# Performance work log

Measured on AMD Instinct MI355X. Metric: run time of the kernel, lower is better.

Reference implementation:

```python
import jax, jax.numpy as jnp
import numpy as np

B, N, C = 8, 3136, 128
NUM_HEADS = 2
HEAD_DIM = C // NUM_HEADS  # 64
SCALE = HEAD_DIM ** -0.5


def setup_inputs() -> dict:
    key = jax.random.key(0)
    ks = jax.random.split(key, 10)
    s = 0.02
    return {
        "x": jax.random.normal(ks[0], (B, N, C), jnp.float32),
        "H": 56,
        "W": 56,
        "relative_pos": jax.random.normal(ks[1], (NUM_HEADS, N, N), jnp.float32),
        "Wq": jax.random.normal(ks[2], (C, C), jnp.float32) * s,
        "bq": jnp.zeros((C,), jnp.float32),
        "Wk": jax.random.normal(ks[3], (C, C), jnp.float32) * s,
        "bk": jnp.zeros((C,), jnp.float32),
        "Wv": jax.random.normal(ks[4], (C, C), jnp.float32) * s,
        "bv": jnp.zeros((C,), jnp.float32),
        "Wp": jax.random.normal(ks[5], (C, C), jnp.float32) * s,
        "bp": jnp.zeros((C,), jnp.float32),
    }


def reference(x, H, W, relative_pos, Wq, bq, Wk, bk, Wv, bv, Wp, bp):
    # x: [B, N, C]; sr_ratio == 1 path of Attention.forward
    b, n, c = x.shape
    h, dh = NUM_HEADS, HEAD_DIM
    # q/k/v projections -> [B, h, N, dh] (torch Linear: x @ W.T + b)
    q = (x @ Wq.T + bq).reshape(b, n, h, dh).transpose(0, 2, 1, 3)
    k = (x @ Wk.T + bk).reshape(b, n, h, dh).transpose(0, 2, 1, 3)
    v = (x @ Wv.T + bv).reshape(b, n, h, dh).transpose(0, 2, 1, 3)
    # scores with additive relative-position bias: [B, h, N, N]
    attn = jnp.einsum("bhnd,bhmd->bhnm", q, k) * SCALE + relative_pos[None]
    attn = jax.nn.softmax(attn, axis=-1)
    # AV -> [B, N, C]
    out = jnp.einsum("bhnm,bhmd->bhnd", attn, v).transpose(0, 2, 1, 3).reshape(b, n, c)
    return out @ Wp.T + bp
```

## Files before the change

kernel.cpp:

```cpp
#include <hip/hip_runtime.h>
#include <hip/hip_fp16.h>

#define N_TOK 3136
#define DH 64
#define NHEAD 2
#define CDIM 128
#define BATCH 8
#define NT 49
#define QK_SCALE 0.18033688011112f
#define LOG2E 1.4426950408889634f

typedef __attribute__((ext_vector_type(8))) short bf16x8;
typedef __attribute__((ext_vector_type(8))) _Float16 f16x8;
typedef __attribute__((ext_vector_type(2))) _Float16 f16x2;
typedef __attribute__((ext_vector_type(2))) __fp16 fp16x2;
typedef __attribute__((ext_vector_type(4))) float f32x4;
typedef __attribute__((ext_vector_type(16))) float f32x16;
typedef __attribute__((ext_vector_type(4))) unsigned short u16x4;
typedef __attribute__((ext_vector_type(4))) unsigned int u32x4;

__device__ __forceinline__ unsigned short f2bf(float f) {
  unsigned int u = __float_as_uint(f);
  u += 0x7fffu + ((u >> 16) & 1u);
  return (unsigned short)(u >> 16);
}

#define MFMA16(a, b, c)    __builtin_amdgcn_mfma_f32_16x16x32_bf16(a, b, c, 0, 0, 0)
#define MFMA32_BF(a, b, c) __builtin_amdgcn_mfma_f32_32x32x16_bf16(a, b, c, 0, 0, 0)
#define MFMA32_F16(a, b, c) __builtin_amdgcn_mfma_f32_32x32x16_f16(a, b, c, 0, 0, 0)

__device__ __forceinline__ void plswap(unsigned& a, unsigned& b) {
  asm volatile("v_permlane32_swap_b32 %0, %1" : "+v"(a), "+v"(b));
}

__device__ __forceinline__ f16x2 pkrtz(float a, float b) {
  union { fp16x2 p; f16x2 h; } cv;
  cv.p = __builtin_amdgcn_cvt_pkrtz(a, b);
  return cv.h;
}

__device__ __forceinline__ float dot2acc(f16x2 pr, float acc) {
#if __has_builtin(__builtin_amdgcn_fdot2)
  union { f16x2 h; fp16x2 p; } c; c.h = pr;
  fp16x2 ones = {(__fp16)1.0f, (__fp16)1.0f};
  return __builtin_amdgcn_fdot2(c.p, ones, acc, false);
#else
  return acc + (float)pr[0] + (float)pr[1];
#endif
}

__device__ __forceinline__ void stage_w(const float* __restrict__ W,
                                        unsigned short (*wsh)[136], int tid) {
  const float4* Wv4 = (const float4*)W;
#pragma unroll
  for (int i = 0; i < 16; ++i) {
    int f = tid + i * 256;
    float4 v = Wv4[f];
    int row = f >> 5, col = (f & 31) << 2;
    u16x4 pk = { f2bf(v.x), f2bf(v.y), f2bf(v.z), f2bf(v.w) };
    *(u16x4*)&wsh[row][col] = pk;
  }
}

__device__ __forceinline__ void mfma_block(const unsigned short (*xs)[136],
                                           const unsigned short (*wsh)[136],
                                           int w, int lk, int lg, f32x4* acc) {
#pragma unroll
  for (int nf = 0; nf < 8; ++nf) acc[nf] = (f32x4){0.f, 0.f, 0.f, 0.f};
#pragma unroll
  for (int kk = 0; kk < 4; ++kk) {
    bf16x8 a = *(const bf16x8*)&xs[w * 16 + lk][kk * 32 + 8 * lg];
#pragma unroll
    for (int nf = 0; nf < 8; ++nf) {
      bf16x8 b = *(const bf16x8*)&wsh[nf * 16 + lk][kk * 32 + 8 * lg];
      acc[nf] = MFMA16(a, b, acc[nf]);
    }
  }
}

__global__ __launch_bounds__(256)
void proj_qkv(const float* __restrict__ x,
              const float* __restrict__ Wq, const float* __restrict__ bq,
              const float* __restrict__ Wk, const float* __restrict__ bk,
              const float* __restrict__ Wv, const float* __restrict__ bv,
              unsigned short* __restrict__ qo, unsigned short* __restrict__ ko,
              unsigned short* __restrict__ vo)
{
  __shared__ __align__(16) unsigned short xs[64][136];
  __shared__ __align__(16) unsigned short wsh[128][136];
  const int tid = threadIdx.x;
  const int m0 = blockIdx.x * 64;
  const int w = tid >> 6, l = tid & 63;
  const int lk = l & 15, lg = l >> 4;

  {
    const float4* Xv = (const float4*)(x + (size_t)m0 * CDIM);
#pragma unroll
    for (int i = 0; i < 8; ++i) {
      int f = tid + i * 256;
      float4 v = Xv[f];
      int row = f >> 5, col = (f & 31) << 2;
      u16x4 pk = { f2bf(v.x), f2bf(v.y), f2bf(v.z), f2bf(v.w) };
      *(u16x4*)&xs[row][col] = pk;
    }
  }
  stage_w(Wq, wsh, tid);
  __syncthreads();

  f32x4 acc[8];

  mfma_block(xs, wsh, w, lk, lg, acc);
#pragma unroll
  for (int reg = 0; reg < 4; ++reg) {
    int row = m0 + w * 16 + 4 * lg + reg;
    int bb = row / N_TOK, tok = row - bb * N_TOK;
#pragma unroll
    for (int nf = 0; nf < 8; ++nf) {
      int col = nf * 16 + lk;
      float val = (acc[nf][reg] + bq[col]) * QK_SCALE;
      qo[((size_t)(bb * NHEAD + (nf >> 2)) * N_TOK + tok) * DH + (col & 63)] = f2bf(val);
    }
  }
  __syncthreads();

  stage_w(Wk, wsh, tid);
  __syncthreads();
  mfma_block(xs, wsh, w, lk, lg, acc);
#pragma unroll
  for (int reg = 0; reg < 4; ++reg) {
    int row = m0 + w * 16 + 4 * lg + reg;
    int bb = row / N_TOK, tok = row - bb * N_TOK;
#pragma unroll
    for (int nf = 0; nf < 8; ++nf) {
      int col = nf * 16 + lk;
      float val = acc[nf][reg] + bk[col];
      ko[((size_t)(bb * NHEAD + (nf >> 2)) * N_TOK + tok) * DH + (col & 63)] = f2bf(val);
    }
  }
  __syncthreads();

  stage_w(Wv, wsh, tid);
  __syncthreads();
  mfma_block(xs, wsh, w, lk, lg, acc);
#pragma unroll
  for (int reg = 0; reg < 4; ++reg) {
    int row = m0 + w * 16 + 4 * lg + reg;
    int bb = row / N_TOK, tok = row - bb * N_TOK;
#pragma unroll
    for (int nf = 0; nf < 8; ++nf) {
      int col = nf * 16 + lk;
      float val = acc[nf][reg] + bv[col];
      size_t idx = ((size_t)(bb * NHEAD + (nf >> 2)) * DH + (col & 63)) * N_TOK + tok;
      vo[idx] = __half_as_ushort(__float2half(val));
    }
  }
}

__global__ __launch_bounds__(256)
void exp_rp(const float* __restrict__ rp, __half* __restrict__ E)
{
  const int hkt = blockIdx.x;
  const int h = hkt / NT, kt = hkt % NT;
  const int q0 = blockIdx.y * 64;
  const int t = threadIdx.x;
  const int kp = t & 63;
  const int qi = t >> 6;

  const int ct = kp >> 5;
  const int kpp = kp & 31;
  const int hi = (kpp >> 2) & 1;
  const int r = (kpp & 3) + ((kpp >> 3) << 2);
  const int didx = hi * 32 + ct * 16 + r;

  const float* src = rp + ((size_t)h * N_TOK + q0) * N_TOK + kt * 64 + kp;
  __half* dst = E + (((size_t)h * NT + kt) * N_TOK + q0) * 64 + didx;

#pragma unroll
  for (int i = 0; i < 16; ++i) {
    int q = qi * 16 + i;
    float v = __expf(src[(size_t)q * N_TOK]);
    dst[(size_t)q * 64] = __float2half(v);
  }
}

__global__ __launch_bounds__(256)
void attn32(const unsigned short* __restrict__ q_ws,
            const unsigned short* __restrict__ k_ws,
            const unsigned short* __restrict__ v_ws,
            const __half* __restrict__ E,
            unsigned short* __restrict__ attn_out)
{
  __shared__ __align__(16) unsigned short LDSU[2][9216];

  const int b = blockIdx.x, qt = blockIdx.y, head = blockIdx.z;
  const int tid = threadIdx.x;
  const int w = tid >> 6, l = tid & 63;
  const int lq = l & 31, hi = l >> 5;

  const size_t bh = ((size_t)b * NHEAD + head) * N_TOK;
  const unsigned short* Kp = k_ws + bh * DH;
  const _Float16* Vt = (const _Float16*)v_ws + bh * DH;

  int qg = qt * 128 + w * 32 + lq;
  if (qg > N_TOK - 1) qg = N_TOK - 1;

  bf16x8 qf[4];
  {
    const unsigned short* qrow = q_ws + (bh + (size_t)qg) * DH + 8 * hi;
#pragma unroll
    for (int ks = 0; ks < 4; ++ks) qf[ks] = *(const bf16x8*)(qrow + 16 * ks);
  }

  const int kr0 = tid >> 3, ku = tid & 7;
  const int kofs = kr0 * 72 + ku * 8;
  const int gk0 = kr0 * DH + ku * 8, gk1 = gk0 + 32 * DH;
  const int gvt0 = kr0 * N_TOK + ku * 8, gvt1 = gvt0 + 32 * N_TOK;

  const __half* Eb = E + (((size_t)head * NT) * N_TOK + (size_t)qg) * DH + hi * 32;

  float lsum = 0.f;
  f32x16 o0, o1;
#pragma unroll
  for (int i = 0; i < 16; ++i) { o0[i] = 0.f; o1[i] = 0.f; }

  bf16x8 kpreA = *(const bf16x8*)(Kp + gk0);
  bf16x8 kpreB = *(const bf16x8*)(Kp + gk1);
  f16x8 vpreA = *(const f16x8*)(Vt + gvt0);
  f16x8 vpreB = *(const f16x8*)(Vt + gvt1);

  u32x4 EwA[4], EwB[4];
  {
    const u32x4* ep = (const u32x4*)Eb;
#pragma unroll
    for (int f = 0; f < 4; ++f) EwA[f] = ep[f];
  }

  *(bf16x8*)&LDSU[0][kofs] = kpreA;
  *(bf16x8*)&LDSU[0][kofs + 32 * 72] = kpreB;
  *(f16x8*)&LDSU[0][4608 + kofs] = vpreA;
  *(f16x8*)&LDSU[0][4608 + kofs + 32 * 72] = vpreB;
  {
    const unsigned short* kn = Kp + (size_t)64 * DH;
    const _Float16* vn = Vt + 64;
    kpreA = *(const bf16x8*)(kn + gk0);
    kpreB = *(const bf16x8*)(kn + gk1);
    vpreA = *(const f16x8*)(vn + gvt0);
    vpreB = *(const f16x8*)(vn + gvt1);
  }
  asm volatile("s_waitcnt lgkmcnt(0)" ::: "memory");
  __builtin_amdgcn_s_barrier();
  asm volatile("" ::: "memory");

#define ATTN_BODY(PH, KT, EW_CUR, EW_NXT, LAST)                               \
  {                                                                           \
    const unsigned short* Kb = &LDSU[PH][0];                                  \
    const unsigned short* Vb = &LDSU[PH][4608];                               \
    unsigned short* Kn = &LDSU[PH ^ 1][0];                                    \
    unsigned short* Vn = &LDSU[PH ^ 1][4608];                                 \
    if (!(LAST)) {                                         \
      const u32x4* ep = (const u32x4*)(Eb + (size_t)((KT) + 1) * (N_TOK * DH)); \
      _Pragma("unroll") for (int f = 0; f < 4; ++f) EW_NXT[f] = ep[f];        \
    }                                                                         \
                                                           \
    f32x16 s0, s1;                                                            \
    _Pragma("unroll") for (int i = 0; i < 16; ++i) { s0[i] = 0.f; s1[i] = 0.f; } \
    __builtin_amdgcn_s_setprio(1);                                            \
    _Pragma("unroll") for (int ks = 0; ks < 4; ++ks) {                        \
      bf16x8 kf0 = *(const bf16x8*)&Kb[lq * 72 + 16 * ks + 8 * hi];           \
      s0 = MFMA32_BF(kf0, qf[ks], s0);                                        \
      bf16x8 kf1 = *(const bf16x8*)&Kb[(32 + lq) * 72 + 16 * ks + 8 * hi];    \
      s1 = MFMA32_BF(kf1, qf[ks], s1);                                        \
    }                                                                         \
    __builtin_amdgcn_s_setprio(0);                                            \
    if (!(LAST)) {            \
      *(bf16x8*)&Kn[kofs] = kpreA;                                            \
      *(bf16x8*)&Kn[kofs + 32 * 72] = kpreB;                                  \
      *(f16x8*)&Vn[kofs] = vpreA;                                             \
      *(f16x8*)&Vn[kofs + 32 * 72] = vpreB;                                   \
      if ((KT) + 2 < NT) {                                                    \
        const unsigned short* kn2 = Kp + (size_t)((KT) + 2) * 64 * DH;        \
        const _Float16* vn2 = Vt + (size_t)((KT) + 2) * 64;                   \
        kpreA = *(const bf16x8*)(kn2 + gk0);                                  \
        kpreB = *(const bf16x8*)(kn2 + gk1);                                  \
        vpreA = *(const f16x8*)(vn2 + gvt0);                                  \
        vpreB = *(const f16x8*)(vn2 + gvt1);                                  \
      }                                                                       \
    }                                                                         \
                                \
    unsigned pw[16];                                                          \
    _Pragma("unroll") for (int f = 0; f < 4; ++f) {                           \
      int rb = (f & 1) * 8;                                                   \
      _Pragma("unroll") for (int i = 0; i < 4; ++i) {                         \
        float a = (f >> 1) ? s1[rb + 2 * i] : s0[rb + 2 * i];                 \
        float c = (f >> 1) ? s1[rb + 2 * i + 1] : s0[rb + 2 * i + 1];         \
        f16x2 pp = pkrtz(__builtin_amdgcn_exp2f(a), __builtin_amdgcn_exp2f(c)); \
        union { unsigned u; f16x2 h; } ec; ec.u = EW_CUR[f][i];               \
        f16x2 pr = pp * ec.h;                                                 \
        lsum = dot2acc(pr, lsum);                                             \
        union { f16x2 h; unsigned u; } pu; pu.h = pr;                         \
        pw[4 * f + i] = pu.u;                                                 \
      }                                                                       \
      plswap(pw[4 * f + 0], pw[4 * f + 2]);                                   \
      plswap(pw[4 * f + 1], pw[4 * f + 3]);                                   \
    }                                                                         \
                                                        \
    __builtin_amdgcn_s_setprio(1);                                            \
    _Pragma("unroll") for (int ks = 0; ks < 4; ++ks) {                        \
      union { unsigned u[4]; f16x8 v; } pf;                                   \
      _Pragma("unroll") for (int i = 0; i < 4; ++i) pf.u[i] = pw[4 * ks + i]; \
      f16x8 vf0 = *(const f16x8*)&Vb[lq * 72 + 16 * ks + 8 * hi];             \
      o0 = MFMA32_F16(vf0, pf.v, o0);                                         \
      f16x8 vf1 = *(const f16x8*)&Vb[(32 + lq) * 72 + 16 * ks + 8 * hi];      \
      o1 = MFMA32_F16(vf1, pf.v, o1);                                         \
    }                                                                         \
    __builtin_amdgcn_s_setprio(0);                                            \
    if (!(LAST)) {                                                            \
      asm volatile("s_waitcnt lgkmcnt(0)" ::: "memory");                      \
      __builtin_amdgcn_s_barrier();                                           \
      asm volatile("" ::: "memory");                                          \
    }                                                                         \
  }

  for (int kt2 = 0; kt2 < (NT - 1) / 2; ++kt2) {
    int kt = 2 * kt2;
    ATTN_BODY(0, kt, EwA, EwB, false);
    ATTN_BODY(1, kt + 1, EwB, EwA, false);
  }
  ATTN_BODY(0, NT - 1, EwA, EwB, true);
#undef ATTN_BODY

  lsum += __shfl_xor(lsum, 32, 64);
  float inv = 1.f / lsum;

  __syncthreads();
  unsigned short* Ot = &LDSU[0][0];
  const int orow = (w * 32 + lq) * 72;
#pragma unroll
  for (int dt = 0; dt < 2; ++dt) {
#pragma unroll
    for (int j = 0; j < 8; ++j) {
      float v0 = (dt ? o1[2 * j] : o0[2 * j]) * inv;
      float v1 = (dt ? o1[2 * j + 1] : o0[2 * j + 1]) * inv;
      unsigned pk;
      asm("v_cvt_pk_bf16_f32 %0, %1, %2" : "=v"(pk) : "v"(v0), "v"(v1));
      int d = ((2 * j) & 3) + 8 * ((2 * j) >> 2) + 4 * hi + 32 * dt;
      *(unsigned*)&Ot[orow + d] = pk;
    }
  }
  __syncthreads();
#pragma unroll
  for (int i = 0; i < 4; ++i) {
    int c = tid + 256 * i;
    int ql = c >> 3, du = c & 7;
    int tok = qt * 128 + ql;
    if (tok < N_TOK) {
      u32x4 val = *(const u32x4*)&Ot[ql * 72 + du * 8];
      *(u32x4*)&attn_out[((size_t)b * N_TOK + tok) * CDIM + head * DH + du * 8] = val;
    }
  }
}

template<bool IN_F32, int OMODE>
__global__ __launch_bounds__(256)
void proj_gemm(const void* __restrict__ Ain, const float* __restrict__ W,
               const float* __restrict__ bias, void* __restrict__ Out,
               float out_scale)
{
  __shared__ __align__(16) unsigned short xs[64][136];
  __shared__ __align__(16) unsigned short wsh[128][136];
  const int tid = threadIdx.x;
  const int m0 = blockIdx.x * 64;
  const int w = tid >> 6, l = tid & 63;
  const int lk = l & 15, lg = l >> 4;

  stage_w(W, wsh, tid);
  if (IN_F32) {
    const float4* Xv = (const float4*)((const float*)Ain + (size_t)m0 * CDIM);
#pragma unroll
    for (int i = 0; i < 8; ++i) {
      int f = tid + i * 256;
      float4 v = Xv[f];
      int row = f >> 5, col = (f & 31) << 2;
      u16x4 pk = { f2bf(v.x), f2bf(v.y), f2bf(v.z), f2bf(v.w) };
      *(u16x4*)&xs[row][col] = pk;
    }
  } else {
    const bf16x8* Xv = (const bf16x8*)((const unsigned short*)Ain + (size_t)m0 * CDIM);
#pragma unroll
    for (int i = 0; i < 4; ++i) {
      int c = tid + i * 256;
      bf16x8 v = Xv[c];
      int row = c >> 4, col = (c & 15) << 3;
      *(bf16x8*)&xs[row][col] = v;
    }
  }
  __syncthreads();

  f32x4 acc[8];
  mfma_block(xs, wsh, w, lk, lg, acc);

#pragma unroll
  for (int reg = 0; reg < 4; ++reg) {
    int row = m0 + w * 16 + 4 * lg + reg;
    int bb = row / N_TOK;
    int tok = row - bb * N_TOK;
#pragma unroll
    for (int nf = 0; nf < 8; ++nf) {
      int col = nf * 16 + lk;
      float val = (acc[nf][reg] + bias[col]) * out_scale;
      if (OMODE == 0) {
        ((float*)Out)[(size_t)row * CDIM + col] = val;
      } else {
        int head = nf >> 2;
        int d = col & 63;
        size_t idx = ((size_t)(bb * NHEAD + head) * N_TOK + tok) * DH + d;
        ((unsigned short*)Out)[idx] = f2bf(val);
      }
    }
  }
}

__global__ __launch_bounds__(256)
void attn_fallback(const unsigned short* __restrict__ q_ws,
                   const unsigned short* __restrict__ k_ws,
                   const unsigned short* __restrict__ v_ws,
                   const float* __restrict__ relpos,
                   unsigned short* __restrict__ attn_out)
{
  __shared__ __align__(16) unsigned short Ks[64][72];
  __shared__ __align__(16) unsigned short Vts[64][72];
  __shared__ __align__(16) unsigned short Ps[4][16][72];

  const int b = blockIdx.x, qt = blockIdx.y, head = blockIdx.z;
  const int tid = threadIdx.x;
  const int w = tid >> 6, l = tid & 63;
  const int lk = l & 15, lg = l >> 4;

  const size_t bh = ((size_t)b * NHEAD + head) * N_TOK;
  const unsigned short* Qp = q_ws + (bh + (size_t)qt * 64) * DH;
  const unsigned short* Kp = k_ws + bh * DH;
  const unsigned short* Vg = v_ws + bh * DH;

  bf16x8 qf0, qf1;
  {
    const unsigned short* qrow = Qp + (size_t)(w * 16 + lk) * DH + 8 * lg;
    qf0 = *(const bf16x8*)qrow;
    qf1 = *(const bf16x8*)(qrow + 32);
  }

  const int kr0 = tid >> 3;
  const int ku = (tid & 7) << 3;
  const int gk0 = kr0 * DH + ku;
  const int gk1 = gk0 + 32 * DH;
  const int vkey = tid & 63;
  const int vd0 = (tid >> 6) << 3;
  const int gv0 = vkey * DH + vd0;
  const int gv1 = gv0 + 32;

  const int qrow0 = qt * 64 + w * 16;
  const float* rpb = relpos + (size_t)head * N_TOK * N_TOK +
                     (size_t)(qrow0 + 4 * lg) * N_TOK + lk;

  float l_run[4] = {0.f, 0.f, 0.f, 0.f};
  f32x4 acc[4];
#pragma unroll
  for (int nf = 0; nf < 4; ++nf) acc[nf] = (f32x4){0.f, 0.f, 0.f, 0.f};

  bf16x8 kpreA = *(const bf16x8*)(Kp + gk0);
  bf16x8 kpreB = *(const bf16x8*)(Kp + gk1);
  bf16x8 vpreA = *(const bf16x8*)(Vg + gv0);
  bf16x8 vpreB = *(const bf16x8*)(Vg + gv1);

  for (int kt = 0; kt < NT; ++kt) {
    float rp[4][4];
#pragma unroll
    for (int r = 0; r < 4; ++r)
#pragma unroll
      for (int ct = 0; ct < 4; ++ct)
        rp[ct][r] = rpb[(size_t)r * N_TOK + kt * 64 + ct * 16];

    asm volatile("s_waitcnt lgkmcnt(0)" ::: "memory");
    __builtin_amdgcn_s_barrier();
    asm volatile("" ::: "memory");

    *(bf16x8*)&Ks[kr0][ku] = kpreA;
    *(bf16x8*)&Ks[kr0 + 32][ku] = kpreB;
#pragma unroll
    for (int j = 0; j < 8; ++j) Vts[vd0 + j][vkey] = ((const unsigned short*)&vpreA)[j];
#pragma unroll
    for (int j = 0; j < 8; ++j) Vts[vd0 + 32 + j][vkey] = ((const unsigned short*)&vpreB)[j];

    if (kt + 1 < NT) {
      const unsigned short* kn = Kp + (size_t)(kt + 1) * 64 * DH;
      const unsigned short* vn = Vg + (size_t)(kt + 1) * 64 * DH;
      kpreA = *(const bf16x8*)(kn + gk0);
      kpreB = *(const bf16x8*)(kn + gk1);
      vpreA = *(const bf16x8*)(vn + gv0);
      vpreB = *(const bf16x8*)(vn + gv1);
    }

    asm volatile("s_waitcnt lgkmcnt(0)" ::: "memory");
    __builtin_amdgcn_s_barrier();
    asm volatile("" ::: "memory");

    f32x4 s[4];
#pragma unroll
    for (int ct = 0; ct < 4; ++ct) s[ct] = (f32x4){0.f, 0.f, 0.f, 0.f};
#pragma unroll
    for (int ct = 0; ct < 4; ++ct) {
      bf16x8 kb0 = *(const bf16x8*)&Ks[ct * 16 + lk][8 * lg];
      s[ct] = MFMA16(qf0, kb0, s[ct]);
      bf16x8 kb1 = *(const bf16x8*)&Ks[ct * 16 + lk][32 + 8 * lg];
      s[ct] = MFMA16(qf1, kb1, s[ct]);
    }

#pragma unroll
    for (int ct = 0; ct < 4; ++ct) {
      float p0 = __builtin_amdgcn_exp2f(fmaf(rp[ct][0], LOG2E, s[ct][0]));
      float p1 = __builtin_amdgcn_exp2f(fmaf(rp[ct][1], LOG2E, s[ct][1]));
      float p2 = __builtin_amdgcn_exp2f(fmaf(rp[ct][2], LOG2E, s[ct][2]));
      float p3 = __builtin_amdgcn_exp2f(fmaf(rp[ct][3], LOG2E, s[ct][3]));
      l_run[0] += p0; l_run[1] += p1; l_run[2] += p2; l_run[3] += p3;
      Ps[w][4 * lg + 0][ct * 16 + lk] = f2bf(p0);
      Ps[w][4 * lg + 1][ct * 16 + lk] = f2bf(p1);
      Ps[w][4 * lg + 2][ct * 16 + lk] = f2bf(p2);
      Ps[w][4 * lg + 3][ct * 16 + lk] = f2bf(p3);
    }

    bf16x8 pa0 = *(const bf16x8*)&Ps[w][lk][8 * lg];
    bf16x8 pa1 = *(const bf16x8*)&Ps[w][lk][32 + 8 * lg];
#pragma unroll
    for (int nf = 0; nf < 4; ++nf) {
      bf16x8 vb0 = *(const bf16x8*)&Vts[nf * 16 + lk][8 * lg];
      acc[nf] = MFMA16(pa0, vb0, acc[nf]);
      bf16x8 vb1 = *(const bf16x8*)&Vts[nf * 16 + lk][32 + 8 * lg];
      acc[nf] = MFMA16(pa1, vb1, acc[nf]);
    }
  }

#pragma unroll
  for (int m = 1; m <= 8; m <<= 1)
#pragma unroll
    for (int r = 0; r < 4; ++r)
      l_run[r] += __shfl_xor(l_run[r], m, 64);

#pragma unroll
  for (int r = 0; r < 4; ++r) {
    int tok = qrow0 + 4 * lg + r;
    float inv = 1.f / l_run[r];
#pragma unroll
    for (int nf = 0; nf < 4; ++nf) {
      attn_out[((size_t)b * N_TOK + tok) * CDIM + head * DH + nf * 16 + lk] =
          f2bf(acc[nf][r] * inv);
    }
  }
}

extern "C" void kernel_launch(void* const* d_in, const int* in_sizes, int n_in,
                              void* d_out, int out_size, void* d_ws, size_t ws_size,
                              hipStream_t stream) {
  (void)in_sizes; (void)n_in; (void)out_size;
  const float* x      = (const float*)d_in[0];
  const float* relpos = (const float*)d_in[3];
  const float* Wq = (const float*)d_in[4];  const float* bq = (const float*)d_in[5];
  const float* Wk = (const float*)d_in[6];  const float* bk = (const float*)d_in[7];
  const float* Wv = (const float*)d_in[8];  const float* bv = (const float*)d_in[9];
  const float* Wp = (const float*)d_in[10]; const float* bp = (const float*)d_in[11];

  const size_t QKV_ELEMS = (size_t)BATCH * NHEAD * N_TOK * DH;
  const size_t E_ELEMS   = (size_t)NHEAD * NT * N_TOK * DH;
  unsigned short* q_ws  = (unsigned short*)d_ws;
  unsigned short* k_ws  = q_ws + QKV_ELEMS;
  unsigned short* v_ws  = k_ws + QKV_ELEMS;
  unsigned short* ao_ws = v_ws + QKV_ELEMS;
  __half* E_ws = (__half*)(ao_ws + QKV_ELEMS);

  const bool big = ws_size >= (4 * QKV_ELEMS + E_ELEMS) * sizeof(unsigned short);

  dim3 blk(256);
  const int MTILES = (BATCH * N_TOK) / 64;

  if (big) {
    proj_qkv<<<MTILES, blk, 0, stream>>>(x, Wq, bq, Wk, bk, Wv, bv, q_ws, k_ws, v_ws);
    exp_rp<<<dim3(NHEAD * NT, N_TOK / 64), blk, 0, stream>>>(relpos, E_ws);
    attn32<<<dim3(BATCH, (N_TOK + 127) / 128, NHEAD), blk, 0, stream>>>(
        q_ws, k_ws, v_ws, E_ws, ao_ws);
  } else {
    proj_gemm<true, 1><<<MTILES, blk, 0, stream>>>((const void*)x, Wq, bq, (void*)q_ws, QK_SCALE);
    proj_gemm<true, 1><<<MTILES, blk, 0, stream>>>((const void*)x, Wk, bk, (void*)k_ws, 1.f);
    proj_gemm<true, 1><<<MTILES, blk, 0, stream>>>((const void*)x, Wv, bv, (void*)v_ws, 1.f);
    attn_fallback<<<dim3(BATCH, N_TOK / 64, NHEAD), blk, 0, stream>>>(
        q_ws, k_ws, v_ws, relpos, ao_ws);
  }

  proj_gemm<false, 0><<<MTILES, blk, 0, stream>>>((const void*)ao_ws, Wp, bp, d_out, 1.f);
}
```

Before: 120.9 us.

## Merge QKV projection with exp(relpos) kernel and halve attention query tile

Folds the exp(relative_pos) precompute into the QKV projection kernel as extra blocks, removing one launch and letting both independent jobs run concurrently. The attention kernel drops from 256 threads and 128 queries per block to 128 threads and 64 queries, raising the grid from 25 to 49 query tiles per batch-head. This removes the padded last tile and improves load balance across CUs. In exchange, each block stages the same K/V tiles for half as many queries, doubling K/V LDS traffic per query, and each thread now issues four loads per tile instead of two.

```diff
diff --git a/kernel.cpp b/kernel.cpp
--- a/kernel.cpp
+++ b/kernel.cpp
@@ -7,6 +7,9 @@
 #define CDIM 128
 #define BATCH 8
 #define NT 49
+#define QT1 49
+#define MTILES ((BATCH * N_TOK) / 64)
+#define EXPBLKS (NHEAD * NT * (N_TOK / 64))
 #define QK_SCALE 0.18033688011112f
 #define LOG2E 1.4426950408889634f
 
@@ -79,16 +82,43 @@
 }
 
 __global__ __launch_bounds__(256)
-void proj_qkv(const float* __restrict__ x,
-              const float* __restrict__ Wq, const float* __restrict__ bq,
-              const float* __restrict__ Wk, const float* __restrict__ bk,
-              const float* __restrict__ Wv, const float* __restrict__ bv,
-              unsigned short* __restrict__ qo, unsigned short* __restrict__ ko,
-              unsigned short* __restrict__ vo)
+void pre_kernel(const float* __restrict__ x,
+                const float* __restrict__ Wq, const float* __restrict__ bq,
+                const float* __restrict__ Wk, const float* __restrict__ bk,
+                const float* __restrict__ Wv, const float* __restrict__ bv,
+                unsigned short* __restrict__ qo, unsigned short* __restrict__ ko,
+                unsigned short* __restrict__ vo,
+                const float* __restrict__ rp, __half* __restrict__ E)
 {
   __shared__ __align__(16) unsigned short xs[64][136];
   __shared__ __align__(16) unsigned short wsh[128][136];
   const int tid = threadIdx.x;
+
+  if (blockIdx.x >= MTILES) {
+    const int eb = blockIdx.x - MTILES;
+    const int hkt = eb % (NHEAD * NT);
+    const int q0 = (eb / (NHEAD * NT)) * 64;
+    const int h = hkt / NT, kt = hkt % NT;
+    const int kp = tid & 63;
+    const int qi = tid >> 6;
+
+    const int ct = kp >> 5;
+    const int kpp = kp & 31;
+    const int hi = (kpp >> 2) & 1;
+    const int r = (kpp & 3) + ((kpp >> 3) << 2);
+    const int didx = hi * 32 + ct * 16 + r;
+
+    const float* src = rp + ((size_t)h * N_TOK + q0) * N_TOK + kt * 64 + kp;
+    __half* dst = E + (((size_t)h * NT + kt) * N_TOK + q0) * 64 + didx;
+#pragma unroll
+    for (int i = 0; i < 16; ++i) {
+      int q = qi * 16 + i;
+      float v = __expf(src[(size_t)q * N_TOK]);
+      dst[(size_t)q * 64] = __float2half(v);
+    }
+    return;
+  }
+
   const int m0 = blockIdx.x * 64;
   const int w = tid >> 6, l = tid & 63;
   const int lk = l & 15, lg = l >> 4;
@@ -156,34 +186,7 @@
   }
 }
 
-__global__ __launch_bounds__(256)
-void exp_rp(const float* __restrict__ rp, __half* __restrict__ E)
-{
-  const int hkt = blockIdx.x;
-  const int h = hkt / NT, kt = hkt % NT;
-  const int q0 = blockIdx.y * 64;
-  const int t = threadIdx.x;
-  const int kp = t & 63;
-  const int qi = t >> 6;
-
-  const int ct = kp >> 5;
-  const int kpp = kp & 31;
-  const int hi = (kpp >> 2) & 1;
-  const int r = (kpp & 3) + ((kpp >> 3) << 2);
-  const int didx = hi * 32 + ct * 16 + r;
-
-  const float* src = rp + ((size_t)h * N_TOK + q0) * N_TOK + kt * 64 + kp;
-  __half* dst = E + (((size_t)h * NT + kt) * N_TOK + q0) * 64 + didx;
-
-#pragma unroll
-  for (int i = 0; i < 16; ++i) {
-    int q = qi * 16 + i;
-    float v = __expf(src[(size_t)q * N_TOK]);
-    dst[(size_t)q * 64] = __float2half(v);
-  }
-}
-
-__global__ __launch_bounds__(256)
+__global__ __launch_bounds__(128)
 void attn32(const unsigned short* __restrict__ q_ws,
             const unsigned short* __restrict__ k_ws,
             const unsigned short* __restrict__ v_ws,
@@ -201,8 +204,7 @@
   const unsigned short* Kp = k_ws + bh * DH;
   const _Float16* Vt = (const _Float16*)v_ws + bh * DH;
 
-  int qg = qt * 128 + w * 32 + lq;
-  if (qg > N_TOK - 1) qg = N_TOK - 1;
+  const int qg = qt * 64 + w * 32 + lq;
 
   bf16x8 qf[4];
   {
@@ -211,10 +213,10 @@
     for (int ks = 0; ks < 4; ++ks) qf[ks] = *(const bf16x8*)(qrow + 16 * ks);
   }
 
-  const int kr0 = tid >> 3, ku = tid & 7;
-  const int kofs = kr0 * 72 + ku * 8;
-  const int gk0 = kr0 * DH + ku * 8, gk1 = gk0 + 32 * DH;
-  const int gvt0 = kr0 * N_TOK + ku * 8, gvt1 = gvt0 + 32 * N_TOK;
+  const int sr = tid >> 3, su = tid & 7;
+  const int kofs = sr * 72 + su * 8;
+  const int gk = sr * DH + su * 8;
+  const int gvt = sr * N_TOK + su * 8;
 
   const __half* Eb = E + (((size_t)head * NT) * N_TOK + (size_t)qg) * DH + hi * 32;
 
@@ -223,10 +225,12 @@
 #pragma unroll
   for (int i = 0; i < 16; ++i) { o0[i] = 0.f; o1[i] = 0.f; }
 
-  bf16x8 kpreA = *(const bf16x8*)(Kp + gk0);
-  bf16x8 kpreB = *(const bf16x8*)(Kp + gk1);
-  f16x8 vpreA = *(const f16x8*)(Vt + gvt0);
-  f16x8 vpreB = *(const f16x8*)(Vt + gvt1);
+  bf16x8 kpre[4]; f16x8 vpre[4];
+#pragma unroll
+  for (int i = 0; i < 4; ++i) {
+    kpre[i] = *(const bf16x8*)(Kp + gk + i * 16 * DH);
+    vpre[i] = *(const f16x8*)(Vt + gvt + i * 16 * N_TOK);
+  }
 
   u32x4 EwA[4], EwB[4];
   {
@@ -235,29 +239,32 @@
     for (int f = 0; f < 4; ++f) EwA[f] = ep[f];
   }
 
-  *(bf16x8*)&LDSU[0][kofs] = kpreA;
-  *(bf16x8*)&LDSU[0][kofs + 32 * 72] = kpreB;
-  *(f16x8*)&LDSU[0][4608 + kofs] = vpreA;
-  *(f16x8*)&LDSU[0][4608 + kofs + 32 * 72] = vpreB;
+#pragma unroll
+  for (int i = 0; i < 4; ++i) {
+    *(bf16x8*)&LDSU[0][kofs + i * 1152] = kpre[i];
+    *(f16x8*)&LDSU[0][4608 + kofs + i * 1152] = vpre[i];
+  }
   {
     const unsigned short* kn = Kp + (size_t)64 * DH;
     const _Float16* vn = Vt + 64;
-    kpreA = *(const bf16x8*)(kn + gk0);
-    kpreB = *(const bf16x8*)(kn + gk1);
-    vpreA = *(const f16x8*)(vn + gvt0);
-    vpreB = *(const f16x8*)(vn + gvt1);
+#pragma unroll
+    for (int i = 0; i < 4; ++i) {
+      kpre[i] = *(const bf16x8*)(kn + gk + i * 16 * DH);
+      vpre[i] = *(const f16x8*)(vn + gvt + i * 16 * N_TOK);
+    }
   }
   asm volatile("s_waitcnt lgkmcnt(0)" ::: "memory");
   __builtin_amdgcn_s_barrier();
   asm volatile("" ::: "memory");
 
-#define ATTN_BODY(PH, KT, EW_CUR, EW_NXT, LAST)                               \
+#define ATTN_BODY(PH, KT, EW_CUR, EW_NXT)                                     \
   {                                                                           \
+    const bool hasNext = (KT) + 1 < NT;                                       \
     const unsigned short* Kb = &LDSU[PH][0];                                  \
     const unsigned short* Vb = &LDSU[PH][4608];                               \
     unsigned short* Kn = &LDSU[PH ^ 1][0];                                    \
     unsigned short* Vn = &LDSU[PH ^ 1][4608];                                 \
-    if (!(LAST)) {                                         \
+    if (hasNext) {                                         \
       const u32x4* ep = (const u32x4*)(Eb + (size_t)((KT) + 1) * (N_TOK * DH)); \
       _Pragma("unroll") for (int f = 0; f < 4; ++f) EW_NXT[f] = ep[f];        \
     }                                                                         \
@@ -272,18 +279,18 @@
       s1 = MFMA32_BF(kf1, qf[ks], s1);                                        \
     }                                                                         \
     __builtin_amdgcn_s_setprio(0);                                            \
-    if (!(LAST)) {            \
-      *(bf16x8*)&Kn[kofs] = kpreA;                                            \
-      *(bf16x8*)&Kn[kofs + 32 * 72] = kpreB;                                  \
-      *(f16x8*)&Vn[kofs] = vpreA;                                             \
-      *(f16x8*)&Vn[kofs + 32 * 72] = vpreB;                                   \
+    if (hasNext) {            \
+      _Pragma("unroll") for (int i = 0; i < 4; ++i) {                         \
+        *(bf16x8*)&Kn[kofs + i * 1152] = kpre[i];                             \
+        *(f16x8*)&Vn[kofs + i * 1152] = vpre[i];                              \
+      }                                                                       \
       if ((KT) + 2 < NT) {                                                    \
         const unsigned short* kn2 = Kp + (size_t)((KT) + 2) * 64 * DH;        \
         const _Float16* vn2 = Vt + (size_t)((KT) + 2) * 64;                   \
-        kpreA = *(const bf16x8*)(kn2 + gk0);                                  \
-        kpreB = *(const bf16x8*)(kn2 + gk1);                                  \
-        vpreA = *(const f16x8*)(vn2 + gvt0);                                  \
-        vpreB = *(const f16x8*)(vn2 + gvt1);                                  \
+        _Pragma("unroll") for (int i = 0; i < 4; ++i) {                       \
+          kpre[i] = *(const bf16x8*)(kn2 + gk + i * 16 * DH);                 \
+          vpre[i] = *(const f16x8*)(vn2 + gvt + i * 16 * N_TOK);              \
+        }                                                                     \
       }                                                                       \
     }                                                                         \
                                 \
@@ -314,7 +321,7 @@
       o1 = MFMA32_F16(vf1, pf.v, o1);                                         \
     }                                                                         \
     __builtin_amdgcn_s_setprio(0);                                            \
-    if (!(LAST)) {                                                            \
+    if (hasNext) {                                                            \
       asm volatile("s_waitcnt lgkmcnt(0)" ::: "memory");                      \
       __builtin_amdgcn_s_barrier();                                           \
       asm volatile("" ::: "memory");                                          \
@@ -323,10 +330,10 @@
 
   for (int kt2 = 0; kt2 < (NT - 1) / 2; ++kt2) {
     int kt = 2 * kt2;
-    ATTN_BODY(0, kt, EwA, EwB, false);
-    ATTN_BODY(1, kt + 1, EwB, EwA, false);
-  }
-  ATTN_BODY(0, NT - 1, EwA, EwB, true);
+    ATTN_BODY(0, kt, EwA, EwB);
+    ATTN_BODY(1, kt + 1, EwB, EwA);
+  }
+  ATTN_BODY(0, NT - 1, EwA, EwB);
 #undef ATTN_BODY
 
   lsum += __shfl_xor(lsum, 32, 64);
@@ -350,13 +357,11 @@
   __syncthreads();
 #pragma unroll
   for (int i = 0; i < 4; ++i) {
-    int c = tid + 256 * i;
+    int c = tid + 128 * i;
     int ql = c >> 3, du = c & 7;
-    int tok = qt * 128 + ql;
-    if (tok < N_TOK) {
-      u32x4 val = *(const u32x4*)&Ot[ql * 72 + du * 8];
-      *(u32x4*)&attn_out[((size_t)b * N_TOK + tok) * CDIM + head * DH + du * 8] = val;
-    }
+    int tok = qt * 64 + ql;
+    u32x4 val = *(const u32x4*)&Ot[ql * 72 + du * 8];
+    *(u32x4*)&attn_out[((size_t)b * N_TOK + tok) * CDIM + head * DH + du * 8] = val;
   }
 }
 
@@ -569,22 +574,22 @@
 
   const size_t QKV_ELEMS = (size_t)BATCH * NHEAD * N_TOK * DH;
   const size_t E_ELEMS   = (size_t)NHEAD * NT * N_TOK * DH;
+
   unsigned short* q_ws  = (unsigned short*)d_ws;
   unsigned short* k_ws  = q_ws + QKV_ELEMS;
   unsigned short* v_ws  = k_ws + QKV_ELEMS;
   unsigned short* ao_ws = v_ws + QKV_ELEMS;
   __half* E_ws = (__half*)(ao_ws + QKV_ELEMS);
 
-  const bool big = ws_size >= (4 * QKV_ELEMS + E_ELEMS) * sizeof(unsigned short);
+  const size_t need_mid = (4 * QKV_ELEMS + E_ELEMS) * sizeof(unsigned short);
 
   dim3 blk(256);
-  const int MTILES = (BATCH * N_TOK) / 64;
-
-  if (big) {
-    proj_qkv<<<MTILES, blk, 0, stream>>>(x, Wq, bq, Wk, bk, Wv, bv, q_ws, k_ws, v_ws);
-    exp_rp<<<dim3(NHEAD * NT, N_TOK / 64), blk, 0, stream>>>(relpos, E_ws);
-    attn32<<<dim3(BATCH, (N_TOK + 127) / 128, NHEAD), blk, 0, stream>>>(
-        q_ws, k_ws, v_ws, E_ws, ao_ws);
+
+  if (ws_size >= need_mid) {
+    pre_kernel<<<MTILES + EXPBLKS, blk, 0, stream>>>(
+        x, Wq, bq, Wk, bk, Wv, bv, q_ws, k_ws, v_ws, relpos, (__half*)E_ws);
+    attn32<<<dim3(BATCH, QT1, NHEAD), dim3(128), 0, stream>>>(
+        q_ws, k_ws, v_ws, (const __half*)E_ws, ao_ws);
   } else {
     proj_gemm<true, 1><<<MTILES, blk, 0, stream>>>((const void*)x, Wq, bq, (void*)q_ws, QK_SCALE);
     proj_gemm<true, 1><<<MTILES, blk, 0, stream>>>((const void*)x, Wk, bk, (void*)k_ws, 1.f);
```

Result: faster. 117.9 us (-2.5%).
